# Kernel tuning notes

Measured on AMD Instinct MI355X. Metric: run time of the kernel, lower is better.

## Reference

```python
import jax, jax.numpy as jnp
import numpy as np

B, N, K, C = 8, 4096, 32, 64
RADIUS = 0.15
CIN = C + 3  # dp_fj: concat(dp[3], fj[C])


def _ball_query(p, radius, k):
    """p: (B,N,3). Returns neighbor indices (B,N,K): first k points (in index
    order) within radius of each query, padded with the first valid neighbor
    (ballquery semantics; query point itself is always index 0 candidate)."""
    sq = jnp.sum(p * p, axis=-1)                                  # (B,N)
    d2 = sq[:, :, None] + sq[:, None, :] - 2.0 * jnp.einsum('bnd,bmd->bnm', p, p)
    n = p.shape[1]
    within = d2 <= radius * radius
    key = jnp.where(within, jnp.arange(n, dtype=jnp.int32)[None, None, :], n)
    order = jnp.argsort(key, axis=-1)[..., :k]                    # (B,N,K)
    valid = jnp.take_along_axis(key, order, axis=-1) < n
    first = order[..., :1]
    return jnp.where(valid, order, first)


def _conv2d_1x1(x, w, b):
    # x: (B,Cin,N,K), w: (Cout,Cin), b: (Cout,)
    return jnp.einsum('oi,bink->bonk', w, x) + b[None, :, None, None]


def _conv1d_1x1(x, w, b):
    # x: (B,Cin,N)
    return jnp.einsum('oi,bin->bon', w, x) + b[None, :, None]


def setup_inputs() -> dict:
    key = jax.random.key(0)
    ks = jax.random.split(key, 16)
    s = 0.05
    inp = {
        'p': jax.random.uniform(ks[0], (B, N, 3), dtype=jnp.float32),
        'f': jax.random.normal(ks[1], (B, C, N), dtype=jnp.float32),
        # attn_local: convblock2d (CIN -> C), no act
        'w_attn': jax.random.normal(ks[2], (C, CIN), dtype=jnp.float32) * s,
        'b_attn': jnp.zeros((C,), jnp.float32),
        # convs: convblock2d (CIN -> C, relu) then (C -> C, no act)
        'w1': jax.random.normal(ks[3], (C, CIN), dtype=jnp.float32) * s,
        'b1': jnp.zeros((C,), jnp.float32),
        'w2': jax.random.normal(ks[4], (C, C), dtype=jnp.float32) * s,
        'b2': jnp.zeros((C,), jnp.float32),
        # ffn: convblock1d (C -> C*expansion=C, relu) then (C -> C, no act)
        'wf1': jax.random.normal(ks[5], (C, C), dtype=jnp.float32) * s,
        'bf1': jnp.zeros((C,), jnp.float32),
        'wf2': jax.random.normal(ks[6], (C, C), dtype=jnp.float32) * s,
        'bf2': jnp.zeros((C,), jnp.float32),
    }
    return inp


def reference(p, f, w_attn, b_attn, w1, b1, w2, b2, wf1, bf1, wf2, bf2):
    bidx = jnp.arange(B)[:, None, None]
    idx = _ball_query(p, RADIUS, K)                               # (B,N,K) int
    pj = p[bidx, idx]                                             # (B,N,K,3)
    dp = (pj - p[:, :, None, :]).transpose(0, 3, 1, 2)            # (B,3,N,K)
    ft = f.transpose(0, 2, 1)                                     # (B,N,C)
    fj = ft[bidx, idx].transpose(0, 3, 1, 2)                      # (B,C,N,K)

    fj_cat = jnp.concatenate([dp, fj], axis=1)                    # (B,CIN,N,K)

    attn = _conv2d_1x1(fj_cat, w_attn, b_attn)                    # (B,C,N,K)
    x = jax.nn.relu(_conv2d_1x1(fj_cat, w1, b1))
    x = _conv2d_1x1(x, w2, b2)                                    # (B,C,N,K)

    # new_attention, 4D path: softmax over neighbor axis (tau=1), weighted sum
    channel_attn = jax.nn.softmax(attn, axis=-1)
    fout = jnp.sum(channel_attn * x, axis=-1)                     # (B,C,N)

    fout = jax.nn.relu(fout + f)
    identity = fout
    h = jax.nn.relu(_conv1d_1x1(fout, wf1, bf1))
    h = _conv1d_1x1(h, wf2, bf2)
    fout = jax.nn.relu(h + identity)                              # use_res
    return (p, fout)
```

## Files before the change

kernel.cpp:

```cpp
#include <hip/hip_runtime.h>

#define B_ 8
#define N_ 4096
#define K_ 32
#define C_ 64
#define CIN_ 67
#define R2_ 0.0225f

#define SFJ 104
#define SY1 72
#define SFB 72
#define PTS 4
#define ITERS 4

typedef short short8v __attribute__((ext_vector_type(8)));
typedef short short4v __attribute__((ext_vector_type(4)));
typedef float floatx4 __attribute__((ext_vector_type(4)));

__device__ __forceinline__ short f2bf(float x) {
    unsigned u = __float_as_uint(x);
    u += 0x7fffu + ((u >> 16) & 1u);
    return (short)(u >> 16);
}

template <int CTRL>
__device__ __forceinline__ float dpp_add(float x) {
    const int m = __builtin_amdgcn_update_dpp(0, __float_as_int(x), CTRL, 0xF, 0xF, false);
    return x + __int_as_float(m);
}
__device__ __forceinline__ float row16_sum(float x) {
    x = dpp_add<0xB1>(x);
    x = dpp_add<0x4E>(x);
    x = dpp_add<0x141>(x);
    x = dpp_add<0x140>(x);
    return x;
}

__global__ __launch_bounds__(256) void prep_kernel(
    const float* __restrict__ p, const float* __restrict__ f,
    unsigned short* __restrict__ ftb, float4* __restrict__ p4,
    float* __restrict__ pout)
{
#pragma clang fp contract(off)
    __shared__ short tile[64 * 72];
    const int t = threadIdx.x;
    const int b = blockIdx.x >> 6;
    const int n0 = (blockIdx.x & 63) * 64;
    const int nn4 = t & 15, ch = t >> 4;
    for (int cc = 0; cc < 4; ++cc) {
        const int c = cc * 16 + ch;
        const float4 v = *(const float4*)&f[((size_t)(b * 64 + c)) * N_ + n0 + nn4 * 4];
        tile[(nn4 * 4 + 0) * 72 + c] = f2bf(v.x);
        tile[(nn4 * 4 + 1) * 72 + c] = f2bf(v.y);
        tile[(nn4 * 4 + 2) * 72 + c] = f2bf(v.z);
        tile[(nn4 * 4 + 3) * 72 + c] = f2bf(v.w);
    }
    if (t < 48) {
        const size_t base = ((size_t)(b * N_ + n0)) * 3;
        ((float4*)(pout + base))[t] = ((const float4*)(p + base))[t];
    }
    if (t < 64) {
        const int n = n0 + t;
        const float x = p[((size_t)(b * N_ + n)) * 3 + 0];
        const float y = p[((size_t)(b * N_ + n)) * 3 + 1];
        const float z = p[((size_t)(b * N_ + n)) * 3 + 2];
        const float sq = (x * x + y * y) + z * z;
        p4[(size_t)b * N_ + n] = make_float4(x, y, z, sq);
    }
    __syncthreads();
    const int nn = t >> 2, cb = (t & 3) * 16;
    uint4* dst = (uint4*)&ftb[((size_t)(b * N_ + n0 + nn)) * 64 + cb];
    const uint4* src = (const uint4*)&tile[nn * 72 + cb];
    dst[0] = src[0];
    dst[1] = src[1];
}

__global__ __launch_bounds__(256) void ball_query_kernel(
    const float4* __restrict__ p4, unsigned short* __restrict__ idx)
{
#pragma clang fp contract(off)
    const int lane = threadIdx.x & 63;
    const int wid = (blockIdx.x * blockDim.x + threadIdx.x) >> 6;
    const int q0 = wid * 4;
    const int b = q0 >> 12;
    const float4* pb = p4 + (size_t)b * N_;

    float4 Q[4];
    #pragma unroll
    for (int q = 0; q < 4; ++q)
        Q[q] = pb[(q0 + q) & (N_ - 1)];
    int count[4] = {0, 0, 0, 0};
    int first[4] = {-1, -1, -1, -1};
    for (int base = 0; base < N_; base += 64) {
        const float4 A = pb[base + lane];
        unsigned long long m[4];
        bool w[4];
        #pragma unroll
        for (int q = 0; q < 4; ++q) {
            const float d2 = (Q[q].w + A.w)
                - 2.0f * ((Q[q].x * A.x + Q[q].y * A.y) + Q[q].z * A.z);
            w[q] = (d2 <= R2_);
            m[q] = __ballot(w[q]);
        }
        const unsigned long long below = (1ull << lane) - 1ull;
        #pragma unroll
        for (int q = 0; q < 4; ++q) {
            if (m[q]) {
                if (first[q] < 0) first[q] = base + __builtin_ctzll(m[q]);
                if (w[q]) {
                    const int pos = count[q] + __popcll(m[q] & below);
                    if (pos < K_)
                        idx[(size_t)(q0 + q) * K_ + pos] = (unsigned short)(base + lane);
                }
                count[q] += __popcll(m[q]);
            }
        }
        if (count[0] >= K_ && count[1] >= K_ && count[2] >= K_ && count[3] >= K_)
            break;
    }
    #pragma unroll
    for (int q = 0; q < 4; ++q)
        for (int pos = count[q] + lane; pos < K_; pos += 64)
            idx[(size_t)(q0 + q) * K_ + pos] = (unsigned short)first[q];
}

__global__ __launch_bounds__(256, 3) void lpa_mfma_kernel(
    const float4* __restrict__ p4, const float* __restrict__ f,
    const unsigned short* __restrict__ ftb,
    const float* __restrict__ w_attn, const float* __restrict__ b_attn,
    const float* __restrict__ w1, const float* __restrict__ b1,
    const float* __restrict__ w2, const float* __restrict__ b2,
    const float* __restrict__ wf1, const float* __restrict__ bf1,
    const float* __restrict__ wf2, const float* __restrict__ bf2,
    const unsigned short* __restrict__ idx, float* __restrict__ out)
{
    __shared__ __align__(16) short s_fj[128 * SFJ];
    __shared__ __align__(16) short s_y1[128 * SY1];
    __shared__ __align__(16) short s_fbuf[2 * 16 * SFB];
    __shared__ float s_vec[PTS * 64];
    short* s_vecbf = s_fbuf;
    short* s_hbf   = s_fbuf + 16 * SFB;

    const int t = threadIdx.x;
    const int lane = t & 63;
    const int mb = t >> 6;
    const int l15 = lane & 15;
    const int quad = lane >> 4;

    short8v wa_f[3], w1_f[3], w2_f[2], wf1_f[2], wf2_f[2];
    {
        const int cm = mb * 16 + l15;
        #pragma unroll
        for (int ks = 0; ks < 3; ++ks) {
            short8v a, bq;
            #pragma unroll
            for (int j = 0; j < 8; ++j) {
                const int ip = ks * 32 + quad * 8 + j;
                float va = 0.0f, vb = 0.0f;
                if (ip < 64)      { va = w_attn[cm * CIN_ + ip + 3];  vb = w1[cm * CIN_ + ip + 3]; }
                else if (ip < 67) { va = w_attn[cm * CIN_ + ip - 64]; vb = w1[cm * CIN_ + ip - 64]; }
                a[j] = f2bf(va); bq[j] = f2bf(vb);
            }
            wa_f[ks] = a; w1_f[ks] = bq;
        }
        #pragma unroll
        for (int ks = 0; ks < 2; ++ks) {
            short8v a, bq, cq;
            #pragma unroll
            for (int j = 0; j < 8; ++j) {
                const int kk = ks * 32 + quad * 8 + j;
                a[j]  = f2bf(w2[cm * 64 + kk]);
                bq[j] = f2bf(wf1[cm * 64 + kk]);
                cq[j] = f2bf(wf2[cm * 64 + kk]);
            }
            w2_f[ks] = a; wf1_f[ks] = bq; wf2_f[ks] = cq;
        }
    }

    const int crow = mb * 16 + quad * 4;
    const float4 bav  = *(const float4*)&b_attn[crow];
    const float4 b1v  = *(const float4*)&b1[crow];
    const float4 b2v  = *(const float4*)&b2[crow];
    const float4 bf1v = *(const float4*)&bf1[crow];
    const float4 bf2v = *(const float4*)&bf2[crow];

    for (int e = t; e < 512; e += 256) {
        const int col = e >> 2, c4 = e & 3;
        *(uint4*)&s_fj[col * SFJ + 72 + c4 * 8] = make_uint4(0u, 0u, 0u, 0u);
    }
    for (int e = t; e < 1152; e += 256) ((unsigned*)s_fbuf)[e] = 0u;

    const int pt00 = blockIdx.x * (PTS * ITERS);
    const int bb = pt00 >> 12;
    const float4* pb = p4 + (size_t)bb * N_;

    for (int itn = 0; itn < ITERS; ++itn) {
        const int pt0 = pt00 + itn * PTS;

        {
            const int col = t >> 1, h = t & 1;
            const int j = idx[(size_t)pt0 * K_ + col];
            const uint4* src = (const uint4*)&ftb[((size_t)(bb * N_ + j)) * 64 + h * 32];
            uint4* dst = (uint4*)&s_fj[col * SFJ + h * 32];
            dst[0] = src[0]; dst[1] = src[1]; dst[2] = src[2]; dst[3] = src[3];
            if (h) {
                const int n = (pt0 + (col >> 5)) & (N_ - 1);
                const float4 Pj = pb[j];
                const float4 Pn = pb[n];
                short8v dp = {};
                dp[0] = f2bf(Pj.x - Pn.x);
                dp[1] = f2bf(Pj.y - Pn.y);
                dp[2] = f2bf(Pj.z - Pn.z);
                *(short8v*)&s_fj[col * SFJ + 64] = dp;
            }
        }
        __syncthreads();

        floatx4 accA[8];
        #pragma unroll
        for (int nt = 0; nt < 8; ++nt) {
            const short* bp = &s_fj[(nt * 16 + l15) * SFJ + quad * 8];
            const short8v fb0 = *(const short8v*)(bp);
            const short8v fb1 = *(const short8v*)(bp + 32);
            const short8v fb2 = *(const short8v*)(bp + 64);
            floatx4 a = {0.f, 0.f, 0.f, 0.f};
            a = __builtin_amdgcn_mfma_f32_16x16x32_bf16(wa_f[0], fb0, a, 0, 0, 0);
            a = __builtin_amdgcn_mfma_f32_16x16x32_bf16(wa_f[1], fb1, a, 0, 0, 0);
            a = __builtin_amdgcn_mfma_f32_16x16x32_bf16(wa_f[2], fb2, a, 0, 0, 0);
            accA[nt] = a;
            floatx4 y = {0.f, 0.f, 0.f, 0.f};
            y = __builtin_amdgcn_mfma_f32_16x16x32_bf16(w1_f[0], fb0, y, 0, 0, 0);
            y = __builtin_amdgcn_mfma_f32_16x16x32_bf16(w1_f[1], fb1, y, 0, 0, 0);
            y = __builtin_amdgcn_mfma_f32_16x16x32_bf16(w1_f[2], fb2, y, 0, 0, 0);
            short4v yp;
            yp[0] = f2bf(fmaxf(y[0] + b1v.x, 0.f));
            yp[1] = f2bf(fmaxf(y[1] + b1v.y, 0.f));
            yp[2] = f2bf(fmaxf(y[2] + b1v.z, 0.f));
            yp[3] = f2bf(fmaxf(y[3] + b1v.w, 0.f));
            *(short4v*)&s_y1[(nt * 16 + l15) * SY1 + crow] = yp;
        }
        __syncthreads();

        floatx4 accX[8];
        #pragma unroll
        for (int nt = 0; nt < 8; ++nt) {
            const short* bp = &s_y1[(nt * 16 + l15) * SY1 + quad * 8];
            const short8v yb0 = *(const short8v*)(bp);
            const short8v yb1 = *(const short8v*)(bp + 32);
            floatx4 x = {0.f, 0.f, 0.f, 0.f};
            x = __builtin_amdgcn_mfma_f32_16x16x32_bf16(w2_f[0], yb0, x, 0, 0, 0);
            x = __builtin_amdgcn_mfma_f32_16x16x32_bf16(w2_f[1], yb1, x, 0, 0, 0);
            accX[nt] = x;
        }

        #pragma unroll
        for (int pi = 0; pi < PTS; ++pi) {
            const int n = (pt0 + pi) & (N_ - 1);
            float fo[4];
            #pragma unroll
            for (int r = 0; r < 4; ++r) {
                const float ba = (r == 0) ? bav.x : (r == 1) ? bav.y : (r == 2) ? bav.z : bav.w;
                const float bx = (r == 0) ? b2v.x : (r == 1) ? b2v.y : (r == 2) ? b2v.z : b2v.w;
                const float e0 = __expf(accA[2 * pi][r] + ba);
                const float e1 = __expf(accA[2 * pi + 1][r] + ba);
                const float se = row16_sum(e0 + e1);
                const float sw = row16_sum(e0 * (accX[2 * pi][r] + bx)
                                         + e1 * (accX[2 * pi + 1][r] + bx));
                const float fres = f[((size_t)(bb * 64 + crow + r)) * N_ + n];
                fo[r] = fmaxf(sw * __builtin_amdgcn_rcpf(se) + fres, 0.f);
            }
            if (l15 == 0) {
                *(float4*)&s_vec[pi * 64 + crow] = make_float4(fo[0], fo[1], fo[2], fo[3]);
                short4v fb;
                fb[0] = f2bf(fo[0]); fb[1] = f2bf(fo[1]);
                fb[2] = f2bf(fo[2]); fb[3] = f2bf(fo[3]);
                *(short4v*)&s_vecbf[pi * SFB + crow] = fb;
            }
        }
        __syncthreads();

        {
            const short8v vb0 = *(const short8v*)&s_vecbf[l15 * SFB + quad * 8];
            const short8v vb1 = *(const short8v*)&s_vecbf[l15 * SFB + 32 + quad * 8];
            floatx4 d = {0.f, 0.f, 0.f, 0.f};
            d = __builtin_amdgcn_mfma_f32_16x16x32_bf16(wf1_f[0], vb0, d, 0, 0, 0);
            d = __builtin_amdgcn_mfma_f32_16x16x32_bf16(wf1_f[1], vb1, d, 0, 0, 0);
            if (l15 < PTS) {
                short4v hb;
                hb[0] = f2bf(fmaxf(d[0] + bf1v.x, 0.f));
                hb[1] = f2bf(fmaxf(d[1] + bf1v.y, 0.f));
                hb[2] = f2bf(fmaxf(d[2] + bf1v.z, 0.f));
                hb[3] = f2bf(fmaxf(d[3] + bf1v.w, 0.f));
                *(short4v*)&s_hbf[l15 * SFB + crow] = hb;
            }
        }
        __syncthreads();

        {
            const short8v hb0 = *(const short8v*)&s_hbf[l15 * SFB + quad * 8];
            const short8v hb1 = *(const short8v*)&s_hbf[l15 * SFB + 32 + quad * 8];
            floatx4 d = {0.f, 0.f, 0.f, 0.f};
            d = __builtin_amdgcn_mfma_f32_16x16x32_bf16(wf2_f[0], hb0, d, 0, 0, 0);
            d = __builtin_amdgcn_mfma_f32_16x16x32_bf16(wf2_f[1], hb1, d, 0, 0, 0);
            if (l15 < PTS) {
                const int n = (pt0 + l15) & (N_ - 1);
                out[((size_t)(bb * 64 + crow + 0)) * N_ + n] =
                    fmaxf(d[0] + bf2v.x + s_vec[l15 * 64 + crow + 0], 0.f);
                out[((size_t)(bb * 64 + crow + 1)) * N_ + n] =
                    fmaxf(d[1] + bf2v.y + s_vec[l15 * 64 + crow + 1], 0.f);
                out[((size_t)(bb * 64 + crow + 2)) * N_ + n] =
                    fmaxf(d[2] + bf2v.z + s_vec[l15 * 64 + crow + 2], 0.f);
                out[((size_t)(bb * 64 + crow + 3)) * N_ + n] =
                    fmaxf(d[3] + bf2v.w + s_vec[l15 * 64 + crow + 3], 0.f);
            }
        }
    }
}

extern "C" void kernel_launch(void* const* d_in, const int* in_sizes, int n_in,
                              void* d_out, int out_size, void* d_ws, size_t ws_size,
                              hipStream_t stream)
{
    const float* p      = (const float*)d_in[0];
    const float* f      = (const float*)d_in[1];
    const float* w_attn = (const float*)d_in[2];
    const float* b_attn = (const float*)d_in[3];
    const float* w1     = (const float*)d_in[4];
    const float* b1     = (const float*)d_in[5];
    const float* w2     = (const float*)d_in[6];
    const float* b2     = (const float*)d_in[7];
    const float* wf1    = (const float*)d_in[8];
    const float* bf1    = (const float*)d_in[9];
    const float* wf2    = (const float*)d_in[10];
    const float* bf2    = (const float*)d_in[11];
    float* out = (float*)d_out;

    unsigned short* idx = (unsigned short*)d_ws;
    unsigned short* ftb = (unsigned short*)((char*)d_ws + 2u * 1024 * 1024);
    float4* p4          = (float4*)((char*)d_ws + 6u * 1024 * 1024);

    prep_kernel<<<B_ * (N_ / 64), 256, 0, stream>>>(p, f, ftb, p4, out);
    ball_query_kernel<<<(B_ * N_) / 16, 256, 0, stream>>>(p4, idx);
    lpa_mfma_kernel<<<(B_ * N_) / (PTS * ITERS), 256, 0, stream>>>(
        p4, f, ftb, w_attn, b_attn, w1, b1, w2, b2, wf1, bf1, wf2, bf2,
        idx, out + (size_t)B_ * N_ * 3);
}
```

Before: 229.2 us.

## Replace brute-force ball query with uniform-grid spatial hashing

Adds a per-batch kernel that bins points into a 6x6x6 uniform grid with a counting sort, storing the sorted points and their original indices. The ball query then scans only the 27 neighbouring cells of each query, one query per wave, instead of sweeping all points in index order. Hits are collected in LDS, and the K smallest indices are picked with a binary search over the index value; first-valid padding uses a min-reduction. The cost is an extra build launch that uses only 8 blocks and a serial prefix scan. Hits beyond a fixed cap of 160 are dropped, and neighbours are no longer written in index order, which is harmless only because the later softmax-weighted sum does not depend on neighbour order.

```diff
diff --git a/kernel.cpp b/kernel.cpp
--- a/kernel.cpp
+++ b/kernel.cpp
@@ -6,6 +6,10 @@
 #define C_ 64
 #define CIN_ 67
 #define R2_ 0.0225f
+
+#define NCELL 6
+#define CELLS 216
+#define HCAP 160
 
 #define SFJ 104
 #define SY1 72
@@ -75,53 +79,123 @@
     dst[1] = src[1];
 }
 
-__global__ __launch_bounds__(256) void ball_query_kernel(
-    const float4* __restrict__ p4, unsigned short* __restrict__ idx)
+__global__ __launch_bounds__(256) void grid_build_kernel(
+    const float* __restrict__ p, float4* __restrict__ sp4,
+    unsigned short* __restrict__ sidx, int* __restrict__ cell_start)
 {
 #pragma clang fp contract(off)
+    __shared__ int hist[CELLS + 1];
+    __shared__ unsigned short cellof[N_];
+    const int t = threadIdx.x;
+    const int b = blockIdx.x;
+    for (int e = t; e <= CELLS; e += 256) hist[e] = 0;
+    __syncthreads();
+    const float* pb = p + (size_t)b * N_ * 3;
+    for (int n = t; n < N_; n += 256) {
+        const int cx = min((int)(pb[n * 3 + 0] * 6.0f), 5);
+        const int cy = min((int)(pb[n * 3 + 1] * 6.0f), 5);
+        const int cz = min((int)(pb[n * 3 + 2] * 6.0f), 5);
+        const int c = (cx * 6 + cy) * 6 + cz;
+        cellof[n] = (unsigned short)c;
+        atomicAdd(&hist[c], 1);
+    }
+    __syncthreads();
+    if (t == 0) {
+        int acc = 0;
+        for (int c = 0; c <= CELLS; ++c) { const int v = hist[c]; hist[c] = acc; acc += v; }
+    }
+    __syncthreads();
+    for (int e = t; e <= CELLS; e += 256)
+        cell_start[b * (CELLS + 1) + e] = hist[e];
+    __syncthreads();
+    for (int n = t; n < N_; n += 256) {
+        const int c = cellof[n];
+        const int pos = atomicAdd(&hist[c], 1);
+        const float x = pb[n * 3 + 0], y = pb[n * 3 + 1], z = pb[n * 3 + 2];
+        const float sq = (x * x + y * y) + z * z;
+        sp4[(size_t)b * N_ + pos] = make_float4(x, y, z, sq);
+        sidx[(size_t)b * N_ + pos] = (unsigned short)n;
+    }
+}
+
+__global__ __launch_bounds__(256) void ball_query_grid_kernel(
+    const float4* __restrict__ p4, const float4* __restrict__ sp4,
+    const unsigned short* __restrict__ sidx, const int* __restrict__ cell_start,
+    unsigned short* __restrict__ idx)
+{
+#pragma clang fp contract(off)
+    __shared__ unsigned short s_hits[4][HCAP];
     const int lane = threadIdx.x & 63;
-    const int wid = (blockIdx.x * blockDim.x + threadIdx.x) >> 6;
-    const int q0 = wid * 4;
-    const int b = q0 >> 12;
-    const float4* pb = p4 + (size_t)b * N_;
-
-    float4 Q[4];
-    #pragma unroll
-    for (int q = 0; q < 4; ++q)
-        Q[q] = pb[(q0 + q) & (N_ - 1)];
-    int count[4] = {0, 0, 0, 0};
-    int first[4] = {-1, -1, -1, -1};
-    for (int base = 0; base < N_; base += 64) {
-        const float4 A = pb[base + lane];
-        unsigned long long m[4];
-        bool w[4];
-        #pragma unroll
-        for (int q = 0; q < 4; ++q) {
-            const float d2 = (Q[q].w + A.w)
-                - 2.0f * ((Q[q].x * A.x + Q[q].y * A.y) + Q[q].z * A.z);
-            w[q] = (d2 <= R2_);
-            m[q] = __ballot(w[q]);
-        }
-        const unsigned long long below = (1ull << lane) - 1ull;
-        #pragma unroll
-        for (int q = 0; q < 4; ++q) {
-            if (m[q]) {
-                if (first[q] < 0) first[q] = base + __builtin_ctzll(m[q]);
-                if (w[q]) {
-                    const int pos = count[q] + __popcll(m[q] & below);
-                    if (pos < K_)
-                        idx[(size_t)(q0 + q) * K_ + pos] = (unsigned short)(base + lane);
-                }
-                count[q] += __popcll(m[q]);
-            }
-        }
-        if (count[0] >= K_ && count[1] >= K_ && count[2] >= K_ && count[3] >= K_)
-            break;
-    }
-    #pragma unroll
-    for (int q = 0; q < 4; ++q)
-        for (int pos = count[q] + lane; pos < K_; pos += 64)
-            idx[(size_t)(q0 + q) * K_ + pos] = (unsigned short)first[q];
+    const int w = threadIdx.x >> 6;
+    const int q = blockIdx.x * 4 + w;
+    const int b = q >> 12;
+    const int n = q & (N_ - 1);
+    const float4 Q = p4[(size_t)b * N_ + n];
+    const int cx = min((int)(Q.x * 6.0f), 5);
+    const int cy = min((int)(Q.y * 6.0f), 5);
+    const int cz = min((int)(Q.z * 6.0f), 5);
+    const int* cs = cell_start + b * (CELLS + 1);
+    const float4* sp = sp4 + (size_t)b * N_;
+    const unsigned short* si = sidx + (size_t)b * N_;
+
+    const int x0 = max(cx - 1, 0), x1 = min(cx + 1, 5);
+    const int y0 = max(cy - 1, 0), y1 = min(cy + 1, 5);
+    const int z0 = max(cz - 1, 0), z1 = min(cz + 1, 5);
+    const unsigned long long below = (1ull << lane) - 1ull;
+
+    int H = 0;
+    for (int xx = x0; xx <= x1; ++xx)
+    for (int yy = y0; yy <= y1; ++yy) {
+        const int rbase = (xx * 6 + yy) * 6;
+        const int beg = cs[rbase + z0];
+        const int end = cs[rbase + z1 + 1];
+        for (int s = beg; s < end; s += 64) {
+            const int i = s + lane;
+            bool hit = false;
+            unsigned short oi = 0;
+            if (i < end) {
+                const float4 A = sp[i];
+                const float d2 = (Q.w + A.w)
+                    - 2.0f * ((Q.x * A.x + Q.y * A.y) + Q.z * A.z);
+                hit = (d2 <= R2_);
+                oi = si[i];
+            }
+            const unsigned long long m = __ballot(hit);
+            if (hit) {
+                const int pos = H + __popcll(m & below);
+                if (pos < HCAP) s_hits[w][pos] = oi;
+            }
+            H += __popcll(m);
+        }
+    }
+    if (H > HCAP) H = HCAP;
+
+    unsigned short* o = idx + (size_t)q * K_;
+    if (H <= K_) {
+        int v = (lane < H) ? (int)s_hits[w][lane] : 0x7FFFFFFF;
+        for (int d = 32; d; d >>= 1) v = min(v, __shfl_xor(v, d));
+        if (lane < K_)
+            o[lane] = (lane < H) ? s_hits[w][lane] : (unsigned short)v;
+    } else {
+        const int h0 = (lane       < H) ? (int)s_hits[w][lane      ] : 0x7FFF;
+        const int h1 = (lane + 64  < H) ? (int)s_hits[w][lane + 64 ] : 0x7FFF;
+        const int h2 = (lane + 128 < H) ? (int)s_hits[w][lane + 128] : 0x7FFF;
+        int lo = 0, hi = N_ - 1;
+        while (lo < hi) {
+            const int mid = (lo + hi) >> 1;
+            int c = (h0 <= mid) + (h1 <= mid) + (h2 <= mid);
+            for (int d = 32; d; d >>= 1) c += __shfl_xor(c, d);
+            if (c >= K_) hi = mid; else lo = mid + 1;
+        }
+        const unsigned long long m0 = __ballot(h0 <= lo);
+        if (h0 <= lo) o[__popcll(m0 & below)] = (unsigned short)h0;
+        int base = __popcll(m0);
+        const unsigned long long m1 = __ballot(h1 <= lo);
+        if (h1 <= lo) o[base + __popcll(m1 & below)] = (unsigned short)h1;
+        base += __popcll(m1);
+        const unsigned long long m2 = __ballot(h2 <= lo);
+        if (h2 <= lo) o[base + __popcll(m2 & below)] = (unsigned short)h2;
+    }
 }
 
 __global__ __launch_bounds__(256, 3) void lpa_mfma_kernel(
@@ -335,12 +409,18 @@
     const float* bf2    = (const float*)d_in[11];
     float* out = (float*)d_out;
 
-    unsigned short* idx = (unsigned short*)d_ws;
-    unsigned short* ftb = (unsigned short*)((char*)d_ws + 2u * 1024 * 1024);
-    float4* p4          = (float4*)((char*)d_ws + 6u * 1024 * 1024);
+    char* ws = (char*)d_ws;
+    unsigned short* ftb  = (unsigned short*)(ws);
+    float4* p4           = (float4*)(ws + 4194304);
+    float4* sp4          = (float4*)(ws + 4718592);
+    unsigned short* sidx = (unsigned short*)(ws + 5242880);
+    int* cell_start      = (int*)(ws + 5308416);
+    unsigned short* idx  = (unsigned short*)(ws + 5505024);
 
     prep_kernel<<<B_ * (N_ / 64), 256, 0, stream>>>(p, f, ftb, p4, out);
-    ball_query_kernel<<<(B_ * N_) / 16, 256, 0, stream>>>(p4, idx);
+    grid_build_kernel<<<B_, 256, 0, stream>>>(p, sp4, sidx, cell_start);
+    ball_query_grid_kernel<<<(B_ * N_) / 4, 256, 0, stream>>>(
+        p4, sp4, sidx, cell_start, idx);
     lpa_mfma_kernel<<<(B_ * N_) / (PTS * ITERS), 256, 0, stream>>>(
         p4, f, ftb, w_attn, b_attn, w1, b1, w2, b2, wf1, bf1, wf2, bf2,
         idx, out + (size_t)B_ * N_ * 3);
```

Result: slower. 235.9 us (+2.9%).

## Fuse prep into ball query and software-pipeline neighbor gathers in main kernel

Applied to the files above, without the earlier changes.

Merges the prep and ball-query kernels into one launch, with ball query reading raw p directly so it no longer depends on p4 written by other blocks. In the main kernel, neighbor indices are loaded up front, and the next iteration's gathered features and point deltas are prefetched into registers during the current MFMA work, then written to LDS afterwards. Residual f loads are also hoisted ahead of the compute. This removes one launch and hides gather latency, at the cost of more registers and redundant point reads in ball query.

```diff
diff --git a/kernel.cpp b/kernel.cpp
--- a/kernel.cpp
+++ b/kernel.cpp
@@ -36,92 +36,101 @@
     return x;
 }
 
-__global__ __launch_bounds__(256) void prep_kernel(
+__global__ __launch_bounds__(256) void prep_bq_kernel(
     const float* __restrict__ p, const float* __restrict__ f,
     unsigned short* __restrict__ ftb, float4* __restrict__ p4,
-    float* __restrict__ pout)
+    float* __restrict__ pout, unsigned short* __restrict__ idx)
 {
 #pragma clang fp contract(off)
     __shared__ short tile[64 * 72];
     const int t = threadIdx.x;
-    const int b = blockIdx.x >> 6;
-    const int n0 = (blockIdx.x & 63) * 64;
-    const int nn4 = t & 15, ch = t >> 4;
-    for (int cc = 0; cc < 4; ++cc) {
-        const int c = cc * 16 + ch;
-        const float4 v = *(const float4*)&f[((size_t)(b * 64 + c)) * N_ + n0 + nn4 * 4];
-        tile[(nn4 * 4 + 0) * 72 + c] = f2bf(v.x);
-        tile[(nn4 * 4 + 1) * 72 + c] = f2bf(v.y);
-        tile[(nn4 * 4 + 2) * 72 + c] = f2bf(v.z);
-        tile[(nn4 * 4 + 3) * 72 + c] = f2bf(v.w);
-    }
-    if (t < 48) {
-        const size_t base = ((size_t)(b * N_ + n0)) * 3;
-        ((float4*)(pout + base))[t] = ((const float4*)(p + base))[t];
-    }
-    if (t < 64) {
-        const int n = n0 + t;
-        const float x = p[((size_t)(b * N_ + n)) * 3 + 0];
-        const float y = p[((size_t)(b * N_ + n)) * 3 + 1];
-        const float z = p[((size_t)(b * N_ + n)) * 3 + 2];
-        const float sq = (x * x + y * y) + z * z;
-        p4[(size_t)b * N_ + n] = make_float4(x, y, z, sq);
-    }
-    __syncthreads();
-    const int nn = t >> 2, cb = (t & 3) * 16;
-    uint4* dst = (uint4*)&ftb[((size_t)(b * N_ + n0 + nn)) * 64 + cb];
-    const uint4* src = (const uint4*)&tile[nn * 72 + cb];
-    dst[0] = src[0];
-    dst[1] = src[1];
-}
-
-__global__ __launch_bounds__(256) void ball_query_kernel(
-    const float4* __restrict__ p4, unsigned short* __restrict__ idx)
-{
-#pragma clang fp contract(off)
-    const int lane = threadIdx.x & 63;
-    const int wid = (blockIdx.x * blockDim.x + threadIdx.x) >> 6;
-    const int q0 = wid * 4;
-    const int b = q0 >> 12;
-    const float4* pb = p4 + (size_t)b * N_;
-
-    float4 Q[4];
-    #pragma unroll
-    for (int q = 0; q < 4; ++q)
-        Q[q] = pb[(q0 + q) & (N_ - 1)];
-    int count[4] = {0, 0, 0, 0};
-    int first[4] = {-1, -1, -1, -1};
-    for (int base = 0; base < N_; base += 64) {
-        const float4 A = pb[base + lane];
-        unsigned long long m[4];
-        bool w[4];
+    const int b = blockIdx.x >> 8;
+    const int slice = blockIdx.x & 255;
+
+    if (slice < 64) {
+        const int n0 = slice * 64;
+        const int nn4 = t & 15, ch = t >> 4;
+        for (int cc = 0; cc < 4; ++cc) {
+            const int c = cc * 16 + ch;
+            const float4 v = *(const float4*)&f[((size_t)(b * 64 + c)) * N_ + n0 + nn4 * 4];
+            tile[(nn4 * 4 + 0) * 72 + c] = f2bf(v.x);
+            tile[(nn4 * 4 + 1) * 72 + c] = f2bf(v.y);
+            tile[(nn4 * 4 + 2) * 72 + c] = f2bf(v.z);
+            tile[(nn4 * 4 + 3) * 72 + c] = f2bf(v.w);
+        }
+        if (t < 48) {
+            const size_t base = ((size_t)(b * N_ + n0)) * 3;
+            ((float4*)(pout + base))[t] = ((const float4*)(p + base))[t];
+        }
+        if (t < 64) {
+            const int n = n0 + t;
+            const float x = p[((size_t)(b * N_ + n)) * 3 + 0];
+            const float y = p[((size_t)(b * N_ + n)) * 3 + 1];
+            const float z = p[((size_t)(b * N_ + n)) * 3 + 2];
+            const float sq = (x * x + y * y) + z * z;
+            p4[(size_t)b * N_ + n] = make_float4(x, y, z, sq);
+        }
+        __syncthreads();
+        const int nn = t >> 2, cb = (t & 3) * 16;
+        uint4* dst = (uint4*)&ftb[((size_t)(b * N_ + n0 + nn)) * 64 + cb];
+        const uint4* src = (const uint4*)&tile[nn * 72 + cb];
+        dst[0] = src[0];
+        dst[1] = src[1];
+    }
+
+    {
+        const int lane = t & 63;
+        const int w = t >> 6;
+        const int qbase = slice * 16 + w * 4;
+        const float* pb = p + (size_t)b * N_ * 3;
+        float qx[4], qy[4], qz[4], sqn[4];
         #pragma unroll
         for (int q = 0; q < 4; ++q) {
-            const float d2 = (Q[q].w + A.w)
-                - 2.0f * ((Q[q].x * A.x + Q[q].y * A.y) + Q[q].z * A.z);
-            w[q] = (d2 <= R2_);
-            m[q] = __ballot(w[q]);
-        }
-        const unsigned long long below = (1ull << lane) - 1ull;
-        #pragma unroll
-        for (int q = 0; q < 4; ++q) {
-            if (m[q]) {
-                if (first[q] < 0) first[q] = base + __builtin_ctzll(m[q]);
-                if (w[q]) {
-                    const int pos = count[q] + __popcll(m[q] & below);
-                    if (pos < K_)
-                        idx[(size_t)(q0 + q) * K_ + pos] = (unsigned short)(base + lane);
+            const int n = qbase + q;
+            qx[q] = pb[n * 3 + 0];
+            qy[q] = pb[n * 3 + 1];
+            qz[q] = pb[n * 3 + 2];
+            sqn[q] = (qx[q] * qx[q] + qy[q] * qy[q]) + qz[q] * qz[q];
+        }
+        int count[4] = {0, 0, 0, 0};
+        int first[4] = {-1, -1, -1, -1};
+        for (int base = 0; base < N_; base += 64) {
+            const int mI = base + lane;
+            const float mx = pb[mI * 3 + 0];
+            const float my = pb[mI * 3 + 1];
+            const float mz = pb[mI * 3 + 2];
+            const float sqm = (mx * mx + my * my) + mz * mz;
+            unsigned long long m[4];
+            bool wi[4];
+            #pragma unroll
+            for (int q = 0; q < 4; ++q) {
+                const float d2 = (sqn[q] + sqm)
+                    - 2.0f * ((qx[q] * mx + qy[q] * my) + qz[q] * mz);
+                wi[q] = (d2 <= R2_);
+                m[q] = __ballot(wi[q]);
+            }
+            const unsigned long long below = (1ull << lane) - 1ull;
+            #pragma unroll
+            for (int q = 0; q < 4; ++q) {
+                if (m[q]) {
+                    if (first[q] < 0) first[q] = base + __builtin_ctzll(m[q]);
+                    if (wi[q]) {
+                        const int pos = count[q] + __popcll(m[q] & below);
+                        if (pos < K_)
+                            idx[(size_t)((b << 12) + qbase + q) * K_ + pos] =
+                                (unsigned short)(base + lane);
+                    }
+                    count[q] += __popcll(m[q]);
                 }
-                count[q] += __popcll(m[q]);
-            }
-        }
-        if (count[0] >= K_ && count[1] >= K_ && count[2] >= K_ && count[3] >= K_)
-            break;
-    }
-    #pragma unroll
-    for (int q = 0; q < 4; ++q)
-        for (int pos = count[q] + lane; pos < K_; pos += 64)
-            idx[(size_t)(q0 + q) * K_ + pos] = (unsigned short)first[q];
+            }
+            if (count[0] >= K_ && count[1] >= K_ && count[2] >= K_ && count[3] >= K_)
+                break;
+        }
+        #pragma unroll
+        for (int q = 0; q < 4; ++q)
+            for (int pos = count[q] + lane; pos < K_; pos += 64)
+                idx[(size_t)((b << 12) + qbase + q) * K_ + pos] = (unsigned short)first[q];
+    }
 }
 
 __global__ __launch_bounds__(256, 3) void lpa_mfma_kernel(
@@ -146,6 +155,8 @@
     const int mb = t >> 6;
     const int l15 = lane & 15;
     const int quad = lane >> 4;
+    const int col = t >> 1;
+    const int gh  = t & 1;
 
     short8v wa_f[3], w1_f[3], w2_f[2], wf1_f[2], wf2_f[2];
     {
@@ -185,8 +196,8 @@
     const float4 bf2v = *(const float4*)&bf2[crow];
 
     for (int e = t; e < 512; e += 256) {
-        const int col = e >> 2, c4 = e & 3;
-        *(uint4*)&s_fj[col * SFJ + 72 + c4 * 8] = make_uint4(0u, 0u, 0u, 0u);
+        const int cc = e >> 2, c4 = e & 3;
+        *(uint4*)&s_fj[cc * SFJ + 72 + c4 * 8] = make_uint4(0u, 0u, 0u, 0u);
     }
     for (int e = t; e < 1152; e += 256) ((unsigned*)s_fbuf)[e] = 0u;
 
@@ -194,27 +205,53 @@
     const int bb = pt00 >> 12;
     const float4* pb = p4 + (size_t)bb * N_;
 
+    int jv[ITERS];
+    #pragma unroll
+    for (int i = 0; i < ITERS; ++i)
+        jv[i] = idx[(size_t)(pt00 + i * PTS) * K_ + col];
+
+    {
+        const uint4* src = (const uint4*)&ftb[((size_t)(bb * N_ + jv[0])) * 64 + gh * 32];
+        uint4* dst = (uint4*)&s_fj[col * SFJ + gh * 32];
+        dst[0] = src[0]; dst[1] = src[1]; dst[2] = src[2]; dst[3] = src[3];
+        if (gh) {
+            const int n = (pt00 + (col >> 5)) & (N_ - 1);
+            const float4 Pj = pb[jv[0]];
+            const float4 Pn = pb[n];
+            short8v dp = {};
+            dp[0] = f2bf(Pj.x - Pn.x);
+            dp[1] = f2bf(Pj.y - Pn.y);
+            dp[2] = f2bf(Pj.z - Pn.z);
+            *(short8v*)&s_fj[col * SFJ + 64] = dp;
+        }
+    }
+
     for (int itn = 0; itn < ITERS; ++itn) {
         const int pt0 = pt00 + itn * PTS;
-
-        {
-            const int col = t >> 1, h = t & 1;
-            const int j = idx[(size_t)pt0 * K_ + col];
-            const uint4* src = (const uint4*)&ftb[((size_t)(bb * N_ + j)) * 64 + h * 32];
-            uint4* dst = (uint4*)&s_fj[col * SFJ + h * 32];
-            dst[0] = src[0]; dst[1] = src[1]; dst[2] = src[2]; dst[3] = src[3];
-            if (h) {
-                const int n = (pt0 + (col >> 5)) & (N_ - 1);
-                const float4 Pj = pb[j];
-                const float4 Pn = pb[n];
-                short8v dp = {};
-                dp[0] = f2bf(Pj.x - Pn.x);
-                dp[1] = f2bf(Pj.y - Pn.y);
-                dp[2] = f2bf(Pj.z - Pn.z);
-                *(short8v*)&s_fj[col * SFJ + 64] = dp;
-            }
-        }
-        __syncthreads();
+        __syncthreads();
+
+        float fres[PTS][4];
+        #pragma unroll
+        for (int pi = 0; pi < PTS; ++pi) {
+            const int n = (pt0 + pi) & (N_ - 1);
+            #pragma unroll
+            for (int r = 0; r < 4; ++r)
+                fres[pi][r] = f[((size_t)(bb * 64 + crow + r)) * N_ + n];
+        }
+
+        uint4 pf0, pf1, pf2, pf3;
+        float4 Pjn, Pnn;
+        const bool havepf = (itn + 1 < ITERS);
+        if (havepf) {
+            const int j = jv[itn + 1];
+            const uint4* src = (const uint4*)&ftb[((size_t)(bb * N_ + j)) * 64 + gh * 32];
+            pf0 = src[0]; pf1 = src[1]; pf2 = src[2]; pf3 = src[3];
+            if (gh) {
+                const int n = (pt0 + PTS + (col >> 5)) & (N_ - 1);
+                Pjn = pb[j];
+                Pnn = pb[n];
+            }
+        }
 
         floatx4 accA[8];
         #pragma unroll
@@ -253,9 +290,20 @@
             accX[nt] = x;
         }
 
+        if (havepf) {
+            uint4* dst = (uint4*)&s_fj[col * SFJ + gh * 32];
+            dst[0] = pf0; dst[1] = pf1; dst[2] = pf2; dst[3] = pf3;
+            if (gh) {
+                short8v dp = {};
+                dp[0] = f2bf(Pjn.x - Pnn.x);
+                dp[1] = f2bf(Pjn.y - Pnn.y);
+                dp[2] = f2bf(Pjn.z - Pnn.z);
+                *(short8v*)&s_fj[col * SFJ + 64] = dp;
+            }
+        }
+
         #pragma unroll
         for (int pi = 0; pi < PTS; ++pi) {
-            const int n = (pt0 + pi) & (N_ - 1);
             float fo[4];
             #pragma unroll
             for (int r = 0; r < 4; ++r) {
@@ -266,8 +314,7 @@
                 const float se = row16_sum(e0 + e1);
                 const float sw = row16_sum(e0 * (accX[2 * pi][r] + bx)
                                          + e1 * (accX[2 * pi + 1][r] + bx));
-                const float fres = f[((size_t)(bb * 64 + crow + r)) * N_ + n];
-                fo[r] = fmaxf(sw * __builtin_amdgcn_rcpf(se) + fres, 0.f);
+                fo[r] = fmaxf(sw * __builtin_amdgcn_rcpf(se) + fres[pi][r], 0.f);
             }
             if (l15 == 0) {
                 *(float4*)&s_vec[pi * 64 + crow] = make_float4(fo[0], fo[1], fo[2], fo[3]);
@@ -335,12 +382,12 @@
     const float* bf2    = (const float*)d_in[11];
     float* out = (float*)d_out;
 
-    unsigned short* idx = (unsigned short*)d_ws;
-    unsigned short* ftb = (unsigned short*)((char*)d_ws + 2u * 1024 * 1024);
-    float4* p4          = (float4*)((char*)d_ws + 6u * 1024 * 1024);
-
-    prep_kernel<<<B_ * (N_ / 64), 256, 0, stream>>>(p, f, ftb, p4, out);
-    ball_query_kernel<<<(B_ * N_) / 16, 256, 0, stream>>>(p4, idx);
+    char* ws = (char*)d_ws;
+    unsigned short* ftb = (unsigned short*)(ws);
+    float4* p4          = (float4*)(ws + 4194304);
+    unsigned short* idx = (unsigned short*)(ws + 4718592);
+
+    prep_bq_kernel<<<B_ * 256, 256, 0, stream>>>(p, f, ftb, p4, out, idx);
     lpa_mfma_kernel<<<(B_ * N_) / (PTS * ITERS), 256, 0, stream>>>(
         p4, f, ftb, w_attn, b_attn, w1, b1, w2, b2, wf1, bf1, wf2, bf2,
         idx, out + (size_t)B_ * N_ * 3);
```

Result: slower. 321.0 us (+40.0%).
